# Kernel tuning notes

Hardware: AMD Instinct MI355X
Metric: run time of the kernel (lower is better)

Reference implementation:

```python
import jax, jax.numpy as jnp
import numpy as np

N, C, T, H, W = 2, 128, 4, 64, 64
NHEAD = 8
HB, WB = 16, 16  # block_size
BNH, BNW = H // HB, W // WB


def setup_inputs() -> dict:
    key = jax.random.key(0)
    ks = jax.random.split(key, 13)
    f = lambda k, sh, s=1.0: jax.random.normal(k, sh, dtype=jnp.float32) * s
    return {
        'q': f(ks[0], (N, C, T, H, W)),
        'k': f(ks[1], (N, C, T, H, W)),
        'v': f(ks[2], (N, C, T, H, W)),
        'pos_q': f(ks[3], (N, C, T, H, W)),
        'pos_k': f(ks[4], (N, C, T, H, W)),
        'w_in_long': f(ks[5], (3 * C, C), 0.05),
        'b_in_long': f(ks[6], (3 * C,), 0.02),
        'w_out_long': f(ks[7], (C, C), 0.05),
        'b_out_long': f(ks[8], (C,), 0.02),
        'w_in_short': f(ks[9], (3 * C, C), 0.05),
        'b_in_short': f(ks[10], (3 * C,), 0.02),
        'w_out_short': f(ks[11], (C, C), 0.05),
        'b_out_short': f(ks[12], (C,), 0.02),
    }


def _mha(q, k, v, w_in, b_in, w_out, b_out):
    # q: (Lq, B, C), k/v: (Lk, B, C); torch nn.MultiheadAttention (eval, no dropout)
    c = q.shape[-1]
    dh = c // NHEAD
    qp = q @ w_in[:c].T + b_in[:c]
    kp = k @ w_in[c:2 * c].T + b_in[c:2 * c]
    vp = v @ w_in[2 * c:].T + b_in[2 * c:]
    Lq, B, _ = qp.shape
    Lk = kp.shape[0]
    qp = qp.reshape(Lq, B, NHEAD, dh) * (1.0 / np.sqrt(dh)).astype(np.float32)
    kp = kp.reshape(Lk, B, NHEAD, dh)
    vp = vp.reshape(Lk, B, NHEAD, dh)
    scores = jnp.einsum('lbhd,mbhd->bhlm', qp, kp)
    attn = jax.nn.softmax(scores, axis=-1)
    out = jnp.einsum('bhlm,mbhd->lbhd', attn, vp).reshape(Lq, B, c)
    return out @ w_out.T + b_out


def _to_long(x, t):
    # (n,c,t,h,w) -> (t*bn_h*bn_w, n*h_b*w_b, c): one pixel per block, attend across blocks
    n, c = x.shape[0], x.shape[1]
    x = x.reshape(n, c, t, BNH, HB, BNW, WB).transpose(2, 3, 5, 0, 4, 6, 1)
    return x.reshape(t * BNH * BNW, n * HB * WB, c)


def _long_to_short(x, t):
    # (t*bn_h*bn_w, n*h_b*w_b, c) -> (t*h_b*w_b, n*bn_h*bn_w, c): attend within block
    c = x.shape[-1]
    x = x.reshape(t, BNH, BNW, -1, HB, WB, c).transpose(0, 4, 5, 3, 1, 2, 6)
    return x.reshape(t * HB * WB, -1, c)


def reference(q, k, v, pos_q, pos_k, w_in_long, b_in_long, w_out_long, b_out_long,
              w_in_short, b_in_short, w_out_short, b_out_short):
    n, c, t_q, h, w = q.shape
    t_k = k.shape[2]
    qb = _to_long(q, t_q)
    kb = _to_long(k, t_k)
    vb = _to_long(v, t_k)
    pqb = _to_long(pos_q, t_q)
    pkb = _to_long(pos_k, t_k)
    # long-range (inter-block) cross attention
    vb = _mha(qb + pqb, kb + pkb, vb, w_in_long, b_in_long, w_out_long, b_out_long)
    vs = _long_to_short(vb, t_q)
    pqs = _long_to_short(pqb, t_q)
    # short-range (intra-block) self attention
    out = _mha(vs + pqs, vs + pqs, vs, w_in_short, b_in_short, w_out_short, b_out_short)
    out = out.reshape(t_q, HB, WB, n, BNH, BNW, c).transpose(3, 6, 0, 4, 1, 5, 2)
    return out.reshape(n, c, t_q, h, w)
```

## Files before the change

### kernel.cpp

```cpp
#include <hip/hip_runtime.h>
#include <hip/hip_bf16.h>

#define CC 128

typedef __attribute__((ext_vector_type(8))) short short8;
typedef __attribute__((ext_vector_type(16))) float f32x16;

union I4S8 { int4 i; short8 s; int2 h[2]; };

__device__ __forceinline__ unsigned short f2bfu(float f) {
  union { float f; unsigned int i; } x; x.f = f;
  unsigned int r = x.i + 0x7fffu + ((x.i >> 16) & 1u);
  return (unsigned short)(r >> 16);
}
__device__ __forceinline__ short f2bfs(float f) { return (short)f2bfu(f); }
__device__ __forceinline__ unsigned int pk2(float a, float b) {
  union { __hip_bfloat162 h; unsigned int u; } c;
  c.h = __float22bfloat162_rn(make_float2(a, b));
  return c.u;
}
__device__ __forceinline__ float bflo(unsigned int u) {
  union { unsigned int i; float f; } x; x.i = u << 16; return x.f;
}
__device__ __forceinline__ float bfhi(unsigned int u) {
  union { unsigned int i; float f; } x; x.i = u & 0xffff0000u; return x.f;
}
__device__ __forceinline__ float exp2_raw(float x) {
#if __has_builtin(__builtin_amdgcn_exp2f)
  return __builtin_amdgcn_exp2f(x);
#else
  float r; asm("v_exp_f32 %0, %1" : "=v"(r) : "v"(x)); return r;
#endif
}
__device__ __forceinline__ f32x16 fzero16() {
  f32x16 z;
#pragma unroll
  for (int i = 0; i < 16; ++i) z[i] = 0.f;
  return z;
}
__device__ __forceinline__ void ld16(const float* p, float* f) {
#pragma unroll
  for (int i = 0; i < 4; ++i) {
    float4 a = *(const float4*)(p + 4 * i);
    f[4*i] = a.x; f[4*i+1] = a.y; f[4*i+2] = a.z; f[4*i+3] = a.w;
  }
}

#define QSC 0.3606737602f

__global__ __launch_bounds__(256) void k_cvtw(
    const float* __restrict__ wil, const float* __restrict__ wol,
    const float* __restrict__ wis, const float* __restrict__ wos,
    short* __restrict__ o) {
  const int idx = (blockIdx.x * 256 + threadIdx.x) * 8;
  const float* src; int off;
  if (idx < 49152)       { src = wil; off = idx; }
  else if (idx < 65536)  { src = wol; off = idx - 49152; }
  else if (idx < 114688) { src = wis; off = idx - 65536; }
  else                   { src = wos; off = idx - 114688; }
  float f[8];
  float4 a = *(const float4*)(src + off), b = *(const float4*)(src + off + 4);
  f[0]=a.x; f[1]=a.y; f[2]=a.z; f[3]=a.w; f[4]=b.x; f[5]=b.y; f[6]=b.z; f[7]=b.w;
  short8 r;
#pragma unroll
  for (int j = 0; j < 8; ++j) r[j] = f2bfs(f[j]);
  *(short8*)(o + idx) = r;
}

__global__ __launch_bounds__(256) void k_proj_long(
    const float* __restrict__ q, const float* __restrict__ k,
    const float* __restrict__ v, const float* __restrict__ pq,
    const float* __restrict__ pk,
    const short* __restrict__ wbf, const float* __restrict__ b_in,
    short* __restrict__ qb, short* __restrict__ kb, short* __restrict__ vb,
    short* __restrict__ pos_ct) {
  __shared__ short XQ[32][132], XK[32][132], XV[32][132];
  const int tid = threadIdx.x;
  const int wid = tid >> 6, lane = tid & 63;
  const int l31 = lane & 31, g = lane >> 5;
  const int tok0 = blockIdx.x * 32;
  const int l = tok0 >> 9, b0 = tok0 & 511;
  const int t = l >> 4, bh = (l >> 2) & 3, bw = l & 3;
  const int nb = b0 >> 8, ph0 = (b0 >> 4) & 15;
  {
    const int c = tid >> 1, half = tid & 1;
    const int h = bh * 16 + ph0 + half, w0 = bw * 16;
    const size_t gb = (((size_t)(nb * CC + c) * 4 + t) << 12) + h * 64 + w0;
    float a[16], p[16];
    ld16(q + gb, a); ld16(pq + gb, p);
    {
      short8 s0, s1;
#pragma unroll
      for (int j = 0; j < 8; ++j) { s0[j] = f2bfs(p[j]); s1[j] = f2bfs(p[8 + j]); }
      short* pd = pos_ct + (size_t)c * 32768 + tok0 + half * 16;
      *(short8*)pd = s0;
      *(short8*)(pd + 8) = s1;
    }
#pragma unroll
    for (int j = 0; j < 16; ++j) XQ[half * 16 + j][c] = f2bfs(a[j] + p[j]);
    ld16(k + gb, a); ld16(pk + gb, p);
#pragma unroll
    for (int j = 0; j < 16; ++j) XK[half * 16 + j][c] = f2bfs(a[j] + p[j]);
    ld16(v + gb, a);
#pragma unroll
    for (int j = 0; j < 16; ++j) XV[half * 16 + j][c] = f2bfs(a[j]);
  }
  __syncthreads();
  for (int i = 0; i < 3; ++i) {
    const int nt = wid + 4 * i;
    const int nch = nt * 32 + l31;
    const int which = nt >> 2;
    const short (*X)[132] = (which == 0) ? XQ : (which == 1) ? XK : XV;
    f32x16 acc = fzero16();
#pragma unroll
    for (int k0 = 0; k0 < 128; k0 += 16) {
      I4S8 af;
      af.h[0] = *(const int2*)&X[l31][k0 + 8 * g];
      af.h[1] = *(const int2*)&X[l31][k0 + 8 * g + 4];
      short8 bf = *(const short8*)(wbf + nch * CC + k0 + 8 * g);
      acc = __builtin_amdgcn_mfma_f32_32x32x16_bf16(af.s, bf, acc, 0, 0, 0);
    }
    const float bias = b_in[nch];
    const int hh = (nch >> 4) & 7, d = nch & 15;
    short* dst = (which == 0) ? qb : (which == 1) ? kb : vb;
    const float sc = (which == 0) ? QSC : 1.0f;
#pragma unroll
    for (int r = 0; r < 16; ++r) {
      const int tt = (r & 3) + 8 * (r >> 2) + 4 * g;
      dst[((size_t)((b0 + tt) * 8 + hh) * 64 + l) * 16 + d] =
          f2bfs((acc[r] + bias) * sc);
    }
  }
}

template<int SEQ, int BATCH>
__global__ __launch_bounds__(256) void k_attn(
    const short* __restrict__ qsp, const short* __restrict__ ksp,
    const short* __restrict__ vsp, short* __restrict__ ao) {
  __shared__ short vt[4][17 * 36];
  __shared__ float comb[2][64][19];
  const int tid = threadIdx.x;
  const int wid = tid >> 6, lane = tid & 63;
  const int l31 = lane & 31, g = lane >> 5;
  const int QG = SEQ / 64;
  const int blk = ((blockIdx.x & 7) << 8) | (blockIdx.x >> 3);
  const int gw = blk * 4 + wid;
  const int kh = gw & 1;
  const int rest = gw >> 1;
  const int pair = rest / QG;
  const int q0 = (rest % QG) * 64;
  const int batch = pair >> 3, hh = pair & 7;
  const size_t pbase = (size_t)pair * (SEQ * 16);
  short* vtw = &vt[wid][0];
  if (lane < 18) *(int*)(vtw + 16 * 36 + 2 * lane) = 0x3F803F80;

  const short8 qf0 = *(const short8*)(qsp + pbase + (size_t)(q0 + l31) * 16 + 8 * g);
  const short8 qf1 = *(const short8*)(qsp + pbase + (size_t)(q0 + 32 + l31) * 16 + 8 * g);

  f32x16 acc0 = fzero16(), acc1 = fzero16();
  const int arow = (l31 < 16) ? l31 : 16;
  const short* vtr = vtw + arow * 36;
  const int kbeg = kh * (SEQ / 2), kend = kbeg + SEQ / 2;

#pragma unroll 2
  for (int k0 = kbeg; k0 < kend; k0 += 32) {
    const short8 kf = *(const short8*)(ksp + pbase + (size_t)(k0 + l31) * 16 + 8 * g);
    const short8 vf = *(const short8*)(vsp + pbase + (size_t)(k0 + l31) * 16 + 8 * g);
#pragma unroll
    for (int j = 0; j < 8; ++j)
      vtw[(8 * g + j) * 36 + l31] = vf[j];

    f32x16 s0 = __builtin_amdgcn_mfma_f32_32x32x16_bf16(kf, qf0, fzero16(), 0, 0, 0);
    f32x16 s1 = __builtin_amdgcn_mfma_f32_32x32x16_bf16(kf, qf1, fzero16(), 0, 0, 0);

    I4S8 pa0, pb0, pa1, pb1;
#pragma unroll
    for (int j = 0; j < 4; ++j) {
      pa0.i[j] = (int)pk2(exp2_raw(s0[2 * j]), exp2_raw(s0[2 * j + 1]));
      pb0.i[j] = (int)pk2(exp2_raw(s0[8 + 2 * j]), exp2_raw(s0[9 + 2 * j]));
    }
#pragma unroll
    for (int j = 0; j < 4; ++j) {
      pa1.i[j] = (int)pk2(exp2_raw(s1[2 * j]), exp2_raw(s1[2 * j + 1]));
      pb1.i[j] = (int)pk2(exp2_raw(s1[8 + 2 * j]), exp2_raw(s1[9 + 2 * j]));
    }

    I4S8 a1, a2;
    a1.h[0] = *(const int2*)(vtr + 4 * g);
    a1.h[1] = *(const int2*)(vtr + 8 + 4 * g);
    a2.h[0] = *(const int2*)(vtr + 16 + 4 * g);
    a2.h[1] = *(const int2*)(vtr + 24 + 4 * g);
    acc0 = __builtin_amdgcn_mfma_f32_32x32x16_bf16(a1.s, pa0.s, acc0, 0, 0, 0);
    acc0 = __builtin_amdgcn_mfma_f32_32x32x16_bf16(a2.s, pb0.s, acc0, 0, 0, 0);
    acc1 = __builtin_amdgcn_mfma_f32_32x32x16_bf16(a1.s, pa1.s, acc1, 0, 0, 0);
    acc1 = __builtin_amdgcn_mfma_f32_32x32x16_bf16(a2.s, pb1.s, acc1, 0, 0, 0);
  }

  const int pi = wid >> 1;
  if (kh == 1) {
#pragma unroll
    for (int r = 0; r < 9; ++r) {
      comb[pi][lane][r] = acc0[r];
      comb[pi][lane][9 + r] = acc1[r];
    }
  }
  __syncthreads();
  if (kh == 1) return;
#pragma unroll
  for (int r = 0; r < 9; ++r) {
    acc0[r] += comb[pi][lane][r];
    acc1[r] += comb[pi][lane][9 + r];
  }

  const float inv0 = 1.0f / acc0[8];
  const float inv1 = 1.0f / acc1[8];
  const int qi = q0 + l31;
  short* dst0 = ao + ((size_t)qi * BATCH + batch) * CC + hh * 16 + 4 * g;
  short* dst1 = ao + ((size_t)(qi + 32) * BATCH + batch) * CC + hh * 16 + 4 * g;
  uint2 o1, o2;
  o1.x = pk2(acc0[0] * inv0, acc0[1] * inv0);
  o1.y = pk2(acc0[2] * inv0, acc0[3] * inv0);
  o2.x = pk2(acc0[4] * inv0, acc0[5] * inv0);
  o2.y = pk2(acc0[6] * inv0, acc0[7] * inv0);
  *(uint2*)dst0 = o1;
  *(uint2*)(dst0 + 8) = o2;
  o1.x = pk2(acc1[0] * inv1, acc1[1] * inv1);
  o1.y = pk2(acc1[2] * inv1, acc1[3] * inv1);
  o2.x = pk2(acc1[4] * inv1, acc1[5] * inv1);
  o2.y = pk2(acc1[6] * inv1, acc1[7] * inv1);
  *(uint2*)dst1 = o1;
  *(uint2*)(dst1 + 8) = o2;
}

__global__ __launch_bounds__(256) void k_mid(
    const short* __restrict__ ao, const short* __restrict__ pos_ct,
    const short* __restrict__ wobf, const float* __restrict__ b_out_l,
    const short* __restrict__ wibf, const float* __restrict__ b_in_s,
    short* __restrict__ qb, short* __restrict__ kb, short* __restrict__ vb) {
  __shared__ short YQK[32][132], YV[32][132];
  const int tid = threadIdx.x;
  const int wid = tid >> 6, lane = tid & 63;
  const int l31 = lane & 31, g = lane >> 5;
  const int tok0 = blockIdx.x * 32;
  const int l = tok0 >> 9, b0 = tok0 & 511;
  const int t = l >> 4, bh = (l >> 2) & 3, bw = l & 3;
  const int nb = b0 >> 8, ph0 = (b0 >> 4) & 15;
  {
    const int nch = wid * 32 + l31;
    f32x16 acc = fzero16();
#pragma unroll
    for (int k0 = 0; k0 < 128; k0 += 16) {
      short8 af = *(const short8*)(ao + (size_t)(tok0 + l31) * CC + k0 + 8 * g);
      short8 bf = *(const short8*)(wobf + nch * CC + k0 + 8 * g);
      acc = __builtin_amdgcn_mfma_f32_32x32x16_bf16(af, bf, acc, 0, 0, 0);
    }
    const float bias = b_out_l[nch];
    float pos[16];
#pragma unroll
    for (int rr = 0; rr < 4; ++rr) {
      int2 pp = *(const int2*)(pos_ct + (size_t)nch * 32768 + tok0 + rr * 8 + 4 * g);
      pos[rr * 4 + 0] = bflo((unsigned int)pp.x);
      pos[rr * 4 + 1] = bfhi((unsigned int)pp.x);
      pos[rr * 4 + 2] = bflo((unsigned int)pp.y);
      pos[rr * 4 + 3] = bfhi((unsigned int)pp.y);
    }
#pragma unroll
    for (int r = 0; r < 16; ++r) {
      const int tt = (r & 3) + 8 * (r >> 2) + 4 * g;
      const float y = acc[r] + bias;
      YV[tt][nch] = f2bfs(y);
      YQK[tt][nch] = f2bfs(y + pos[r]);
    }
  }
  __syncthreads();
  const int bs = nb * 16 + bh * 4 + bw;
  const int ls0 = (t * 16 + ph0) * 16;
  for (int i = 0; i < 3; ++i) {
    const int nt = wid + 4 * i;
    const int nch = nt * 32 + l31;
    const int which = nt >> 2;
    const short (*X)[132] = (which == 2) ? YV : YQK;
    f32x16 acc = fzero16();
#pragma unroll
    for (int k0 = 0; k0 < 128; k0 += 16) {
      I4S8 af;
      af.h[0] = *(const int2*)&X[l31][k0 + 8 * g];
      af.h[1] = *(const int2*)&X[l31][k0 + 8 * g + 4];
      short8 bf = *(const short8*)(wibf + nch * CC + k0 + 8 * g);
      acc = __builtin_amdgcn_mfma_f32_32x32x16_bf16(af.s, bf, acc, 0, 0, 0);
    }
    const float bias = b_in_s[nch];
    const int hh = (nch >> 4) & 7, d = nch & 15;
    short* dst = (which == 0) ? qb : (which == 1) ? kb : vb;
    const float sc = (which == 0) ? QSC : 1.0f;
    const size_t base = ((size_t)(bs * 8 + hh) * 1024 + ls0) * 16 + d;
#pragma unroll
    for (int r = 0; r < 16; ++r) {
      const int tt = (r & 3) + 8 * (r >> 2) + 4 * g;
      dst[base + (size_t)tt * 16] = f2bfs((acc[r] + bias) * sc);
    }
  }
}

__global__ __launch_bounds__(256) void k_out_short(
    const short* __restrict__ ao, const short* __restrict__ wbf,
    const float* __restrict__ b_out, float* __restrict__ out) {
  const int tid = threadIdx.x;
  const int wid = tid >> 6, lane = tid & 63;
  const int l31 = lane & 31, g = lane >> 5;
  const int bs = blockIdx.x & 31;
  const int qi0 = (blockIdx.x >> 5) << 5;
  const int nb = bs >> 4, bh = (bs >> 2) & 3, bw = bs & 3;
  const int t = qi0 >> 8, ph0 = (qi0 >> 4) & 15;
  const int nch = wid * 32 + l31;
  f32x16 acc = fzero16();
#pragma unroll
  for (int k0 = 0; k0 < 128; k0 += 16) {
    short8 af = *(const short8*)(ao + ((size_t)(qi0 + l31) * 32 + bs) * CC + k0 + 8 * g);
    short8 bf = *(const short8*)(wbf + nch * CC + k0 + 8 * g);
    acc = __builtin_amdgcn_mfma_f32_32x32x16_bf16(af, bf, acc, 0, 0, 0);
  }
  const float bias = b_out[nch];
#pragma unroll
  for (int rr = 0; rr < 4; ++rr) {
    const int tt0 = rr * 8 + 4 * g;
    const int ph_off = tt0 >> 4, pw = tt0 & 15;
    const int h = bh * 16 + ph0 + ph_off, w = bw * 16 + pw;
    const size_t adr = (((size_t)(nb * CC + nch) * 4 + t) << 12) + h * 64 + w;
    float4 f;
    f.x = acc[rr * 4 + 0] + bias; f.y = acc[rr * 4 + 1] + bias;
    f.z = acc[rr * 4 + 2] + bias; f.w = acc[rr * 4 + 3] + bias;
    *(float4*)(out + adr) = f;
  }
}

extern "C" void kernel_launch(void* const* d_in, const int* in_sizes, int n_in,
                              void* d_out, int out_size, void* d_ws, size_t ws_size,
                              hipStream_t stream) {
  (void)in_sizes; (void)n_in; (void)out_size; (void)ws_size;
  const float* q   = (const float*)d_in[0];
  const float* k   = (const float*)d_in[1];
  const float* v   = (const float*)d_in[2];
  const float* pq  = (const float*)d_in[3];
  const float* pk  = (const float*)d_in[4];
  const float* wil = (const float*)d_in[5];
  const float* bil = (const float*)d_in[6];
  const float* wol = (const float*)d_in[7];
  const float* bol = (const float*)d_in[8];
  const float* wis = (const float*)d_in[9];
  const float* bis = (const float*)d_in[10];
  const float* wos = (const float*)d_in[11];
  const float* bos = (const float*)d_in[12];

  short* qs     = (short*)d_ws;
  short* ksb    = qs + 4194304;
  short* vsb    = ksb + 4194304;
  short* ao     = vsb + 4194304;
  short* pos_ct = ao + 4194304;
  short* wbf    = pos_ct + 4194304;

  k_cvtw<<<dim3(64), dim3(256), 0, stream>>>(wil, wol, wis, wos, wbf);
  k_proj_long<<<dim3(1024), dim3(256), 0, stream>>>(q, k, v, pq, pk, wbf, bil,
                                                    qs, ksb, vsb, pos_ct);
  k_attn<64, 512><<<dim3(2048), dim3(256), 0, stream>>>(qs, ksb, vsb, ao);
  k_mid<<<dim3(1024), dim3(256), 0, stream>>>(ao, pos_ct, wbf + 49152, bol,
                                              wbf + 65536, bis, qs, ksb, vsb);
  k_attn<1024, 32><<<dim3(2048), dim3(256), 0, stream>>>(qs, ksb, vsb, ao);
  k_out_short<<<dim3(1024), dim3(256), 0, stream>>>(ao, wbf + 114688, bos,
                                                    (float*)d_out);
}
```

Baseline: 143.3 us.

## Double-buffer V staging in attention, drop split-K for short sequences, remap projection loads

```diff
diff --git a/kernel.cpp b/kernel.cpp
--- a/kernel.cpp
+++ b/kernel.cpp
@@ -38,12 +38,9 @@
   for (int i = 0; i < 16; ++i) z[i] = 0.f;
   return z;
 }
-__device__ __forceinline__ void ld16(const float* p, float* f) {
-#pragma unroll
-  for (int i = 0; i < 4; ++i) {
-    float4 a = *(const float4*)(p + 4 * i);
-    f[4*i] = a.x; f[4*i+1] = a.y; f[4*i+2] = a.z; f[4*i+3] = a.w;
-  }
+__device__ __forceinline__ void ld8f(const float* p, float* f) {
+  float4 a = *(const float4*)p, b = *(const float4*)(p + 4);
+  f[0]=a.x; f[1]=a.y; f[2]=a.z; f[3]=a.w; f[4]=b.x; f[5]=b.y; f[6]=b.z; f[7]=b.w;
 }
 
 #define QSC 0.3606737602f
@@ -59,8 +56,7 @@
   else if (idx < 114688) { src = wis; off = idx - 65536; }
   else                   { src = wos; off = idx - 114688; }
   float f[8];
-  float4 a = *(const float4*)(src + off), b = *(const float4*)(src + off + 4);
-  f[0]=a.x; f[1]=a.y; f[2]=a.z; f[3]=a.w; f[4]=b.x; f[5]=b.y; f[6]=b.z; f[7]=b.w;
+  ld8f(src + off, f);
   short8 r;
 #pragma unroll
   for (int j = 0; j < 8; ++j) r[j] = f2bfs(f[j]);
@@ -83,27 +79,38 @@
   const int t = l >> 4, bh = (l >> 2) & 3, bw = l & 3;
   const int nb = b0 >> 8, ph0 = (b0 >> 4) & 15;
   {
-    const int c = tid >> 1, half = tid & 1;
-    const int h = bh * 16 + ph0 + half, w0 = bw * 16;
-    const size_t gb = (((size_t)(nb * CC + c) * 4 + t) << 12) + h * 64 + w0;
-    float a[16], p[16];
-    ld16(q + gb, a); ld16(pq + gb, p);
-    {
-      short8 s0, s1;
-#pragma unroll
-      for (int j = 0; j < 8; ++j) { s0[j] = f2bfs(p[j]); s1[j] = f2bfs(p[8 + j]); }
-      short* pd = pos_ct + (size_t)c * 32768 + tok0 + half * 16;
-      *(short8*)pd = s0;
-      *(short8*)(pd + 8) = s1;
-    }
-#pragma unroll
-    for (int j = 0; j < 16; ++j) XQ[half * 16 + j][c] = f2bfs(a[j] + p[j]);
-    ld16(k + gb, a); ld16(pk + gb, p);
-#pragma unroll
-    for (int j = 0; j < 16; ++j) XK[half * 16 + j][c] = f2bfs(a[j] + p[j]);
-    ld16(v + gb, a);
-#pragma unroll
-    for (int j = 0; j < 16; ++j) XV[half * 16 + j][c] = f2bfs(a[j]);
+    const int p = tid & 63;
+    const int seg = tid >> 6;
+    const int h = bh * 16 + ph0 + (seg >> 1);
+    const int w0 = bw * 16 + (seg & 1) * 8;
+    const int j0 = seg * 8;
+    float aq[2][8], ak[2][8], av[2][8], pp0[2][8];
+#pragma unroll
+    for (int cc = 0; cc < 2; ++cc) {
+      const int c = 2 * p + cc;
+      const size_t gb = (((size_t)(nb * CC + c) * 4 + t) << 12) + h * 64 + w0;
+      float a[8], pp[8];
+      ld8f(q + gb, a); ld8f(pq + gb, pp);
+#pragma unroll
+      for (int j = 0; j < 8; ++j) { aq[cc][j] = a[j] + pp[j]; pp0[cc][j] = pp[j]; }
+      ld8f(k + gb, a); ld8f(pk + gb, pp);
+#pragma unroll
+      for (int j = 0; j < 8; ++j) ak[cc][j] = a[j] + pp[j];
+      ld8f(v + gb, av[cc]);
+    }
+#pragma unroll
+    for (int cc = 0; cc < 2; ++cc) {
+      short8 s;
+#pragma unroll
+      for (int j = 0; j < 8; ++j) s[j] = f2bfs(pp0[cc][j]);
+      *(short8*)(pos_ct + (size_t)(2 * p + cc) * 32768 + tok0 + j0) = s;
+    }
+#pragma unroll
+    for (int j = 0; j < 8; ++j) {
+      *(int*)&XQ[j0 + j][2 * p] = (int)pk2(aq[0][j], aq[1][j]);
+      *(int*)&XK[j0 + j][2 * p] = (int)pk2(ak[0][j], ak[1][j]);
+      *(int*)&XV[j0 + j][2 * p] = (int)pk2(av[0][j], av[1][j]);
+    }
   }
   __syncthreads();
   for (int i = 0; i < 3; ++i) {
@@ -133,42 +140,54 @@
   }
 }
 
-template<int SEQ, int BATCH>
+template<int SEQ, int BATCH, int SPLITK>
 __global__ __launch_bounds__(256) void k_attn(
     const short* __restrict__ qsp, const short* __restrict__ ksp,
     const short* __restrict__ vsp, short* __restrict__ ao) {
-  __shared__ short vt[4][17 * 36];
+  __shared__ short vt[4][2][17 * 36];
   __shared__ float comb[2][64][19];
   const int tid = threadIdx.x;
   const int wid = tid >> 6, lane = tid & 63;
   const int l31 = lane & 31, g = lane >> 5;
-  const int QG = SEQ / 64;
-  const int blk = ((blockIdx.x & 7) << 8) | (blockIdx.x >> 3);
+  constexpr int QG = SEQ / 64;
+  constexpr int NBLK = (BATCH * 8 * QG * SPLITK) / 4;
+  const int blk = (blockIdx.x & 7) * (NBLK / 8) + (blockIdx.x >> 3);
   const int gw = blk * 4 + wid;
-  const int kh = gw & 1;
-  const int rest = gw >> 1;
+  const int kh = (SPLITK == 2) ? (gw & 1) : 0;
+  const int rest = (SPLITK == 2) ? (gw >> 1) : gw;
   const int pair = rest / QG;
   const int q0 = (rest % QG) * 64;
   const int batch = pair >> 3, hh = pair & 7;
   const size_t pbase = (size_t)pair * (SEQ * 16);
-  short* vtw = &vt[wid][0];
-  if (lane < 18) *(int*)(vtw + 16 * 36 + 2 * lane) = 0x3F803F80;
+  short* vtw0 = &vt[wid][0][0];
+  short* vtw1 = &vt[wid][1][0];
+  if (lane < 18) {
+    *(int*)(vtw0 + 16 * 36 + 2 * lane) = 0x3F803F80;
+    *(int*)(vtw1 + 16 * 36 + 2 * lane) = 0x3F803F80;
+  }
 
   const short8 qf0 = *(const short8*)(qsp + pbase + (size_t)(q0 + l31) * 16 + 8 * g);
   const short8 qf1 = *(const short8*)(qsp + pbase + (size_t)(q0 + 32 + l31) * 16 + 8 * g);
 
   f32x16 acc0 = fzero16(), acc1 = fzero16();
   const int arow = (l31 < 16) ? l31 : 16;
-  const short* vtr = vtw + arow * 36;
-  const int kbeg = kh * (SEQ / 2), kend = kbeg + SEQ / 2;
-
-#pragma unroll 2
-  for (int k0 = kbeg; k0 < kend; k0 += 32) {
-    const short8 kf = *(const short8*)(ksp + pbase + (size_t)(k0 + l31) * 16 + 8 * g);
-    const short8 vf = *(const short8*)(vsp + pbase + (size_t)(k0 + l31) * 16 + 8 * g);
-#pragma unroll
-    for (int j = 0; j < 8; ++j)
-      vtw[(8 * g + j) * 36 + l31] = vf[j];
+  const short* vtr0 = vtw0 + arow * 36;
+  const short* vtr1 = vtw1 + arow * 36;
+  constexpr int NT = SEQ / 32 / SPLITK;
+  const int t0 = kh * NT;
+
+  auto stage = [&](int kt, short* buf) {
+    const short8 vf =
+        *(const short8*)(vsp + pbase + (size_t)(kt * 32 + l31) * 16 + 8 * g);
+#pragma unroll
+    for (int j = 0; j < 8; ++j) buf[(8 * g + j) * 36 + l31] = vf[j];
+  };
+  stage(t0, vtw0);
+
+  for (int tt = 0; tt < NT; ++tt) {
+    const short8 kf =
+        *(const short8*)(ksp + pbase + (size_t)((t0 + tt) * 32 + l31) * 16 + 8 * g);
+    if (tt + 1 < NT) stage(t0 + tt + 1, ((tt + 1) & 1) ? vtw1 : vtw0);
 
     f32x16 s0 = __builtin_amdgcn_mfma_f32_32x32x16_bf16(kf, qf0, fzero16(), 0, 0, 0);
     f32x16 s1 = __builtin_amdgcn_mfma_f32_32x32x16_bf16(kf, qf1, fzero16(), 0, 0, 0);
@@ -185,6 +204,7 @@
       pb1.i[j] = (int)pk2(exp2_raw(s1[8 + 2 * j]), exp2_raw(s1[9 + 2 * j]));
     }
 
+    const short* vtr = (tt & 1) ? vtr1 : vtr0;
     I4S8 a1, a2;
     a1.h[0] = *(const int2*)(vtr + 4 * g);
     a1.h[1] = *(const int2*)(vtr + 8 + 4 * g);
@@ -196,20 +216,22 @@
     acc1 = __builtin_amdgcn_mfma_f32_32x32x16_bf16(a2.s, pb1.s, acc1, 0, 0, 0);
   }
 
-  const int pi = wid >> 1;
-  if (kh == 1) {
+  if (SPLITK == 2) {
+    const int pi = wid >> 1;
+    if (kh == 1) {
+#pragma unroll
+      for (int r = 0; r < 9; ++r) {
+        comb[pi][lane][r] = acc0[r];
+        comb[pi][lane][9 + r] = acc1[r];
+      }
+    }
+    __syncthreads();
+    if (kh == 1) return;
 #pragma unroll
     for (int r = 0; r < 9; ++r) {
-      comb[pi][lane][r] = acc0[r];
-      comb[pi][lane][9 + r] = acc1[r];
-    }
-  }
-  __syncthreads();
-  if (kh == 1) return;
-#pragma unroll
-  for (int r = 0; r < 9; ++r) {
-    acc0[r] += comb[pi][lane][r];
-    acc1[r] += comb[pi][lane][9 + r];
+      acc0[r] += comb[pi][lane][r];
+      acc1[r] += comb[pi][lane][9 + r];
+    }
   }
 
   const float inv0 = 1.0f / acc0[8];
@@ -362,10 +384,10 @@
   k_cvtw<<<dim3(64), dim3(256), 0, stream>>>(wil, wol, wis, wos, wbf);
   k_proj_long<<<dim3(1024), dim3(256), 0, stream>>>(q, k, v, pq, pk, wbf, bil,
                                                     qs, ksb, vsb, pos_ct);
-  k_attn<64, 512><<<dim3(2048), dim3(256), 0, stream>>>(qs, ksb, vsb, ao);
+  k_attn<64, 512, 1><<<dim3(1024), dim3(256), 0, stream>>>(qs, ksb, vsb, ao);
   k_mid<<<dim3(1024), dim3(256), 0, stream>>>(ao, pos_ct, wbf + 49152, bol,
                                               wbf + 65536, bis, qs, ksb, vsb);
-  k_attn<1024, 32><<<dim3(2048), dim3(256), 0, stream>>>(qs, ksb, vsb, ao);
+  k_attn<1024, 32, 2><<<dim3(2048), dim3(256), 0, stream>>>(qs, ksb, vsb, ao);
   k_out_short<<<dim3(1024), dim3(256), 0, stream>>>(ao, wbf + 114688, bos,
                                                     (float*)d_out);
 }
```

New measurement: 145.8 us. No clear change (+1.8%).
